# Performance work log

Hardware: AMD Instinct MI355X
Metric: run time of the kernel (lower is better)

## Reference

```python
import math
import jax, jax.numpy as jnp
import numpy as np
from jax import lax

# FPN anchor layout: 1024x768 image, strides {4,8,16,32,64}, 3 anchors/location
NUM_PER_LEVEL = (147456, 36864, 9216, 2304, 576)
A_TOTAL = sum(NUM_PER_LEVEL)
BATCH = 8
PRE_NMS_TOP_N = 1000   # testing
POST_NMS_TOP_N = 1000  # testing
NMS_THRESH = 0.7
SCORE_THRESH = 0.0
MIN_SIZE = 1.0
IMG_H, IMG_W = 768.0, 1024.0
BBOX_XFORM_CLIP = math.log(1000.0 / 16.0)


def setup_inputs() -> dict:
    key = jax.random.key(0)
    k1, k2, k3, k4, k5, k6 = jax.random.split(key, 6)
    objectness = jax.random.normal(k1, (BATCH, A_TOTAL), jnp.float32)
    pred_bbox_deltas = jax.random.normal(k2, (BATCH, A_TOTAL, 4), jnp.float32) * 0.2
    # valid anchor boxes (x1, y1, x2, y2)
    cx = jax.random.uniform(k3, (A_TOTAL,), jnp.float32) * IMG_W
    cy = jax.random.uniform(k4, (A_TOTAL,), jnp.float32) * IMG_H
    w = 16.0 + jax.random.uniform(k5, (A_TOTAL,), jnp.float32) * 176.0
    h = 16.0 + jax.random.uniform(k6, (A_TOTAL,), jnp.float32) * 176.0
    anchors = jnp.stack([cx - 0.5 * w, cy - 0.5 * h, cx + 0.5 * w, cy + 0.5 * h], -1)
    return {"objectness": objectness, "pred_bbox_deltas": pred_bbox_deltas, "anchors": anchors}


def _nms_image(boxes, scores, lvl, valid):
    """batched_nms (level-offset trick) + post-NMS top-k, fixed shapes.
    boxes [K,4], scores [K], lvl [K] int, valid [K] bool -> [POST_NMS_TOP_N, 5]"""
    K = boxes.shape[0]
    s = jnp.where(valid, scores, -1.0)
    order = jnp.argsort(-s)  # decreasing score (invalid last)
    b = boxes[order]
    s = s[order]
    v = valid[order]
    # offset boxes per level so cross-level boxes never overlap (torchvision batched_nms)
    offset = lvl[order].astype(b.dtype) * (jnp.max(lax.stop_gradient(boxes)) + 1.0)
    nb = lax.stop_gradient(b) + offset[:, None]
    area = (nb[:, 2] - nb[:, 0]) * (nb[:, 3] - nb[:, 1])
    lt = jnp.maximum(nb[:, None, :2], nb[None, :, :2])  # [K,K,2]
    rb = jnp.minimum(nb[:, None, 2:], nb[None, :, 2:])
    wh = jnp.clip(rb - lt, 0.0)
    inter = wh[..., 0] * wh[..., 1]
    iou = inter / jnp.maximum(area[:, None] + area[None, :] - inter, 1e-9)
    pos = jnp.arange(K)

    def body(keep, i):
        sup = keep[i] & (iou[i] > NMS_THRESH) & (pos > i)
        return keep & ~sup, None

    keep, _ = lax.scan(body, v, pos)
    masked = jnp.where(keep, s, -1.0)
    top_s, top_i = lax.top_k(masked, POST_NMS_TOP_N)  # kept, decreasing score
    sel_b = b[top_i]
    ok = top_s > -0.5
    sel_b = jnp.where(ok[:, None], sel_b, 0.0)
    top_s = jnp.where(ok, top_s, 0.0)
    return jnp.concatenate([sel_b, top_s[:, None]], axis=-1)


def reference(objectness, pred_bbox_deltas, anchors):
    # --- box decode (BoxCoder, weights (1,1,1,1)) ---
    wa = anchors[:, 2] - anchors[:, 0]
    ha = anchors[:, 3] - anchors[:, 1]
    cxa = anchors[:, 0] + 0.5 * wa
    cya = anchors[:, 1] + 0.5 * ha
    dx, dy = pred_bbox_deltas[..., 0], pred_bbox_deltas[..., 1]
    dw = jnp.minimum(pred_bbox_deltas[..., 2], BBOX_XFORM_CLIP)
    dh = jnp.minimum(pred_bbox_deltas[..., 3], BBOX_XFORM_CLIP)
    pcx = dx * wa + cxa
    pcy = dy * ha + cya
    pw = jnp.exp(dw) * wa
    ph = jnp.exp(dh) * ha
    proposals = jnp.stack(
        [pcx - 0.5 * pw, pcy - 0.5 * ph, pcx + 0.5 * pw, pcy + 0.5 * ph], axis=-1
    )  # [B, A, 4]

    # --- per-level pre-NMS top-k (_get_top_n_idx) ---
    levels = jnp.concatenate(
        [jnp.full((n,), i, jnp.int32) for i, n in enumerate(NUM_PER_LEVEL)]
    )
    idx_parts = []
    off = 0
    for n in NUM_PER_LEVEL:
        k = min(PRE_NMS_TOP_N, n)
        _, ti = lax.top_k(objectness[:, off:off + n], k)
        idx_parts.append(ti + off)
        off += n
    top_idx = jnp.concatenate(idx_parts, axis=1)  # [B, K]

    scores = jax.nn.sigmoid(jnp.take_along_axis(objectness, top_idx, axis=1))
    lvl = levels[top_idx]
    boxes = jnp.take_along_axis(proposals, top_idx[..., None], axis=1)  # [B,K,4]

    # --- clip to image ---
    x1 = jnp.clip(boxes[..., 0], 0.0, IMG_W)
    y1 = jnp.clip(boxes[..., 1], 0.0, IMG_H)
    x2 = jnp.clip(boxes[..., 2], 0.0, IMG_W)
    y2 = jnp.clip(boxes[..., 3], 0.0, IMG_H)
    boxes = jnp.stack([x1, y1, x2, y2], axis=-1)

    # remove_small_boxes + score threshold (as validity mask; fixed shapes)
    valid = ((x2 - x1) >= MIN_SIZE) & ((y2 - y1) >= MIN_SIZE) & (scores >= SCORE_THRESH)

    # --- per-image batched NMS + post-NMS top-k ---
    return jax.vmap(_nms_image)(boxes, scores, lvl, valid)  # [B, POST_NMS_TOP_N, 5]
```

## Files before the change

kernel.cpp:

```cpp
#include <hip/hip_runtime.h>
#include <math.h>

#pragma clang fp contract(off)

#define A_TOTAL 196416
#define BATCH 8
#define KTOT 4576
#define NLEV 5
#define MSPLIT 16
#define RCAP 6144
#define NPARTS 12

static __device__ const int d_aoff[NLEV] = {0, 147456, 184320, 193536, 195840};
static __device__ const int d_n[NLEV]    = {147456, 36864, 9216, 2304, 576};
static __device__ const int d_k[NLEV]    = {1000, 1000, 1000, 1000, 576};
static __device__ const int d_spl[NLEV]  = {8, 2, 1, 1, 1};
static __device__ const int d_bp[NLEV]   = {0, 8, 10, 11, 12};
static __device__ const int d_pb_l[13]    = {0,0,0,0,0,0,0,0,1,1,2,3,4};
static __device__ const int d_pb_part[13] = {0,1,2,3,4,5,6,7,0,1,0,0,0};

#define TM_IOU (0.699999988079071044921875 + 0x1p-25)

__device__ inline unsigned int mono(float f) {
  unsigned int u = __float_as_uint(f);
  return (u & 0x80000000u) ? ~u : (u | 0x80000000u);
}
__device__ inline float imono(unsigned int m) {
  return __uint_as_float((m & 0x80000000u) ? (m & 0x7FFFFFFFu) : ~m);
}

__device__ inline int cnt_gt(const float* A, int n, float s) {
  int lo = 0, hi = n;
  while (lo < hi) { int mid = (lo + hi) >> 1; if (A[mid] > s) lo = mid + 1; else hi = mid; }
  return lo;
}
__device__ inline int cnt_ge(const float* A, int n, float s) {
  int lo = 0, hi = n;
  while (lo < hi) { int mid = (lo + hi) >> 1; if (A[mid] >= s) lo = mid + 1; else hi = mid; }
  return lo;
}

__global__ __launch_bounds__(1024) void k_hist(const float* __restrict__ obj,
                                               int* __restrict__ hist_g,
                                               int* __restrict__ cnt_g,
                                               float* __restrict__ maxblk,
                                               float* __restrict__ out) {
  int blk = blockIdx.x;
  int tid = threadIdx.x;
  if (blk == 0) {
    for (int i = tid; i < 40 * NPARTS; i += 1024) maxblk[i] = 0.0f;
    for (int i = tid; i < 40; i += 1024) cnt_g[i] = 0;
  }
  int b = blk / 13, pb = blk % 13;
  if (pb == 0) {
    float* ob = out + (size_t)b * 5000;
    for (int i = tid; i < 5000; i += 1024) ob[i] = 0.0f;
  }
  int l = d_pb_l[pb], part = d_pb_part[pb];
  int slice = d_n[l] / d_spl[l];
  int start = d_aoff[l] + part * slice;
  const float4* p4 = (const float4*)(obj + (size_t)b * A_TOTAL + start);
  int s4 = slice >> 2;
  __shared__ int h[4096];
  for (int i = tid; i < 4096; i += 1024) h[i] = 0;
  __syncthreads();
  for (int i = tid; i < s4; i += 1024) {
    float4 v = p4[i];
    atomicAdd(&h[mono(v.x) >> 20], 1);
    atomicAdd(&h[mono(v.y) >> 20], 1);
    atomicAdd(&h[mono(v.z) >> 20], 1);
    atomicAdd(&h[mono(v.w) >> 20], 1);
  }
  __syncthreads();
  int* outp = hist_g + (size_t)blk * 4096;
  for (int i = tid; i < 4096; i += 1024) outp[i] = h[i];
}

__global__ __launch_bounds__(1024) void k_collect(const float* __restrict__ obj,
                                                  const int* __restrict__ hist_g,
                                                  int* __restrict__ cnt_g,
                                                  unsigned long long* __restrict__ cand_g) {
  int blk = blockIdx.x;
  int b = blk / 13, pb = blk % 13;
  int l = d_pb_l[pb], part = d_pb_part[pb];
  int bl = b * NLEV + l;
  const int k = d_k[l];
  int tid = threadIdx.x, lane = tid & 63;
  __shared__ int t[4096];
  __shared__ int grp[256];
  __shared__ unsigned int sP;
  __shared__ __align__(16) unsigned long long lbuf[RCAP];
  __shared__ int s_cnt, s_base;
  int parts = d_spl[l];
  const int* hb = hist_g + (size_t)(b * 13 + d_bp[l]) * 4096;
  for (int bin = tid; bin < 4096; bin += 1024) {
    int s = 0;
    for (int p = 0; p < parts; ++p) s += hb[p * 4096 + bin];
    t[bin] = s;
  }
  if (tid == 0) s_cnt = 0;
  __syncthreads();
  if (tid < 256) {
    int s = 0;
    for (int j = 0; j < 16; ++j) s += t[tid * 16 + j];
    grp[tid] = s;
  }
  __syncthreads();
  if (tid == 0) {
    int cum = 0, g, d;
    for (g = 255; g >= 0; --g) {
      if (cum + grp[g] >= k) break;
      cum += grp[g];
    }
    for (d = 15; d >= 0; --d) {
      int c = t[g * 16 + d];
      if (cum + c >= k) break;
      cum += c;
    }
    sP = (unsigned int)(g * 16 + d);
  }
  __syncthreads();
  unsigned int P = sP;
  int slice = d_n[l] / parts;
  int start = d_aoff[l] + part * slice;
  const float4* p4 = (const float4*)(obj + (size_t)b * A_TOTAL + start);
  int s4 = slice >> 2;
  int lbase = part * slice;
  for (int i = tid; i < s4; i += 1024) {
    float4 v = p4[i];
    unsigned int a[4] = {mono(v.x), mono(v.y), mono(v.z), mono(v.w)};
    bool q0 = (a[0] >> 20) >= P, q1 = (a[1] >> 20) >= P;
    bool q2 = (a[2] >> 20) >= P, q3 = (a[3] >> 20) >= P;
    if (__ballot(q0 | q1 | q2 | q3)) {
      bool qs[4] = {q0, q1, q2, q3};
#pragma unroll
      for (int c = 0; c < 4; ++c) {
        unsigned long long mb = __ballot(qs[c]);
        if (mb) {
          int base;
          if (lane == 0) base = atomicAdd(&s_cnt, __popcll(mb));
          base = __shfl(base, 0);
          if (qs[c]) {
            int slot = base + __popcll(mb & ((1ull << lane) - 1ull));
            if (slot < RCAP) {
              int idx = lbase + 4 * i + c;
              lbuf[slot] = ((unsigned long long)a[c] << 32) |
                           (unsigned int)(~(unsigned int)idx);
            }
          }
        }
      }
    }
  }
  __syncthreads();
  int cnt = min(s_cnt, RCAP);
  if (tid == 0) s_base = atomicAdd(&cnt_g[bl], cnt);
  __syncthreads();
  int base = s_base;
  for (int i = tid; i < cnt; i += 1024) {
    int slot = base + i;
    if (slot < RCAP) cand_g[(size_t)bl * RCAP + slot] = lbuf[i];
  }
}

__device__ inline float decode_emit(unsigned long long e, int rank, int b,
                                    int k, int aoff, int bl,
                                    const float* __restrict__ deltas,
                                    const float* __restrict__ anchors,
                                    float* __restrict__ sc0,
                                    float4* __restrict__ box0) {
  if (rank >= k) return 0.0f;
  unsigned int k32 = (unsigned int)(e >> 32);
  unsigned int idx = ~(unsigned int)(e & 0xFFFFFFFFull);
  float o = imono(k32);
  int gidx = aoff + (int)idx;
  const float* dl = deltas + ((size_t)b * A_TOTAL + gidx) * 4;
  const float* an = anchors + (size_t)gidx * 4;
  float a0 = an[0], a1 = an[1], a2 = an[2], a3 = an[3];
  float wa = a2 - a0, ha = a3 - a1;
  float cxa = a0 + 0.5f * wa, cya = a1 + 0.5f * ha;
  float dx = dl[0], dy = dl[1];
  const float CLIPV = 4.135166556742356f;
  float dw = fminf(dl[2], CLIPV), dh = fminf(dl[3], CLIPV);
  float pcx = dx * wa + cxa;
  float pcy = dy * ha + cya;
  float pw = (float)exp((double)dw) * wa;
  float ph = (float)exp((double)dh) * ha;
  float x1 = pcx - 0.5f * pw, y1 = pcy - 0.5f * ph;
  float x2 = pcx + 0.5f * pw, y2 = pcy + 0.5f * ph;
  x1 = fminf(fmaxf(x1, 0.0f), 1024.0f);
  x2 = fminf(fmaxf(x2, 0.0f), 1024.0f);
  y1 = fminf(fmaxf(y1, 0.0f), 768.0f);
  y2 = fminf(fmaxf(y2, 0.0f), 768.0f);
  float s = (float)(1.0 / (1.0 + exp(-(double)o)));
  bool valid = ((x2 - x1) >= 1.0f) && ((y2 - y1) >= 1.0f) && (s >= 0.0f);
  sc0[bl * 1024 + rank] = valid ? s : -1.0f;
  box0[bl * 1024 + rank] = make_float4(x1, y1, x2, y2);
  return fmaxf(fmaxf(x1, y1), fmaxf(x2, y2));
}

__global__ __launch_bounds__(256) void k_rankdec(const unsigned long long* __restrict__ cand_g,
                                                 const int* __restrict__ cnt_g,
                                                 const float* __restrict__ deltas,
                                                 const float* __restrict__ anchors,
                                                 float* __restrict__ sc0,
                                                 float4* __restrict__ box0,
                                                 float* __restrict__ maxblk) {
  int bl = blockIdx.x / NPARTS, part = blockIdx.x % NPARTS;
  int b = bl / NLEV, l = bl % NLEV;
  const int k = d_k[l], aoff = d_aoff[l];
  int cnt = min(cnt_g[bl], RCAP);
  if (part * 512 >= cnt) return;
  __shared__ __align__(16) unsigned long long cb[RCAP];
  __shared__ unsigned int s_max;
  int tid = threadIdx.x;
  if (tid == 0) s_max = 0u;
  const unsigned long long* src = cand_g + (size_t)bl * RCAP;
  {
    const ulonglong2* s2 = (const ulonglong2*)src;
    ulonglong2* d2 = (ulonglong2*)cb;
    int n2 = cnt >> 1;
    for (int i = tid; i < n2; i += 256) d2[i] = s2[i];
    if ((cnt & 1) && tid == 0) cb[cnt - 1] = src[cnt - 1];
  }
  __syncthreads();
  int i0 = part * 512 + tid, i1 = i0 + 256;
  unsigned long long e0 = ~0ull, e1 = ~0ull;
  if (i0 < cnt) e0 = cb[i0];
  if (i1 < cnt) e1 = cb[i1];
  int r0 = 0, r1 = 0;
  int nc2 = cnt >> 1;
  const ulonglong2* c2 = (const ulonglong2*)cb;
  for (int j = 0; j < nc2; ++j) {
    ulonglong2 v = c2[j];
    r0 += (v.x > e0) + (v.y > e0);
    r1 += (v.x > e1) + (v.y > e1);
  }
  if (cnt & 1) {
    unsigned long long v = cb[cnt - 1];
    r0 += (v > e0);
    r1 += (v > e1);
  }
  float mx = 0.0f;
  if (i0 < cnt) mx = fmaxf(mx, decode_emit(e0, r0, b, k, aoff, bl, deltas, anchors, sc0, box0));
  if (i1 < cnt) mx = fmaxf(mx, decode_emit(e1, r1, b, k, aoff, bl, deltas, anchors, sc0, box0));
#pragma unroll
  for (int s = 1; s < 64; s <<= 1) mx = fmaxf(mx, __shfl_xor(mx, s));
  if ((tid & 63) == 0) atomicMax(&s_max, __float_as_uint(mx));
  __syncthreads();
  if (tid == 0) maxblk[blockIdx.x] = __uint_as_float(s_max);
}

__global__ __launch_bounds__(1024) void k_mask(const float* __restrict__ sc0,
                                               const float4* __restrict__ box0,
                                               const float* __restrict__ maxblk,
                                               float* __restrict__ lvlsc,
                                               float4* __restrict__ lvlraw,
                                               int* __restrict__ g_V,
                                               unsigned long long* __restrict__ masks) {
  int blk = blockIdx.x;
  int bl = blk / MSPLIT, part = blk % MSPLIT;
  int b = bl / NLEV, l = bl % NLEV;
  const int k = d_k[l];
  int tid = threadIdx.x, lane = tid & 63, w = tid >> 6;
  __shared__ float4 lbox[1024];
  __shared__ float s_mv;
  __shared__ int s_wcnt[16];
  if (w == 0) {
    float v = 0.0f;
    for (int i = lane; i < NLEV * NPARTS; i += 64)
      v = fmaxf(v, maxblk[b * (NLEV * NPARTS) + i]);
#pragma unroll
    for (int s = 1; s < 64; s <<= 1) v = fmaxf(v, __shfl_xor(v, s));
    if (lane == 0) s_mv = v;
  }
  bool in = tid < k;
  float s = in ? sc0[bl * 1024 + tid] : -1.0f;
  bool valid = in && (s >= 0.0f);
  unsigned long long mb = __ballot(valid);
  if (lane == 0) s_wcnt[w] = __popcll(mb);
  __syncthreads();
  int pre = 0;
  for (int ww = 0; ww < w; ++ww) pre += s_wcnt[ww];
  int j = pre + __popcll(mb & ((1ull << lane) - 1ull));
  int V = 0;
  for (int ww = 0; ww < 16; ++ww) V += s_wcnt[ww];
  float off = (float)l * (s_mv + 1.0f);
  if (valid) {
    float4 bx = box0[bl * 1024 + tid];
    lbox[j] = make_float4(bx.x + off, bx.y + off, bx.z + off, bx.w + off);
    if (part == 0) {
      lvlsc[bl * 1024 + j] = s;
      lvlraw[bl * 1024 + j] = bx;
    }
  }
  if (part == 0 && tid == 0) g_V[bl] = V;
  __syncthreads();
  int row0 = part * 64;
  if (row0 >= V) return;
  int i = row0 + lane;
  if (i >= V) return;
  float4 bb = lbox[i];
  float ba = (bb.z - bb.x) * (bb.w - bb.y);
  unsigned long long bits = 0ull;
  int jbase = w * 64;
  if (jbase + 63 > i && jbase < V) {
    int jhi = min(64, V - jbase);
    for (int jo = 0; jo < jhi; ++jo) {
      int jj = jbase + jo;
      float4 cb = lbox[jj];
      float ca = (cb.z - cb.x) * (cb.w - cb.y);
      float xx1 = fmaxf(bb.x, cb.x), yy1 = fmaxf(bb.y, cb.y);
      float xx2 = fminf(bb.z, cb.z), yy2 = fminf(bb.w, cb.w);
      float wd = fmaxf(xx2 - xx1, 0.0f), ht = fmaxf(yy2 - yy1, 0.0f);
      float inter = wd * ht;
      float denom = fmaxf(ba + ca - inter, 1e-9f);
      if ((jj > i) && ((double)inter >= TM_IOU * (double)denom)) bits |= (1ull << jo);
    }
  }
  masks[((size_t)bl * 16 + w) * 1024 + i] = bits;
}

__global__ __launch_bounds__(1024) void k_scan(const unsigned long long* __restrict__ masks,
                                               const int* __restrict__ g_V,
                                               const float* __restrict__ lvlsc,
                                               float* __restrict__ ksc_g,
                                               int* __restrict__ kj_g,
                                               int* __restrict__ K_g) {
  int bl = blockIdx.x;
  int tid = threadIdx.x, lane = tid & 63, w = tid >> 6;
  int V = g_V[bl];
  const int nch = (V + 63) / 64;
  const unsigned long long* M = masks + (size_t)bl * 16 * 1024;
  __shared__ unsigned long long s_remv[16];
  __shared__ unsigned long long s_D[2][72];
  __shared__ unsigned long long s_dw;
  __shared__ int s_wcnt[16];
  if (tid < 16) s_remv[tid] = ~0ull;
  int base_w = w * 64;
  unsigned long long init_w;
  if (V <= base_w) init_w = ~0ull;
  else if (V >= base_w + 64) init_w = 0ull;
  else init_w = (~0ull) << (V - base_w);
  if (w == 0 && nch > 0) s_D[0][lane] = (lane < V) ? M[lane] : 0ull;
  if (tid < 8) { s_D[0][64 + tid] = 0ull; s_D[1][64 + tid] = 0ull; }
  unsigned long long acc = 0ull;
  unsigned long long val_next = 0ull;
  if (w > 0 && w < nch && lane < V) val_next = M[(size_t)w * 1024 + lane];
  __syncthreads();

  for (int c = 0; c < nch; ++c) {
    unsigned long long val = val_next;
    val_next = 0ull;
    int rn = 64 * (c + 1) + lane;
    if (w > c + 1 && w < nch && rn < V) val_next = M[(size_t)w * 1024 + rn];
    if (w == c) {
      unsigned long long red = acc;
#pragma unroll
      for (int s = 1; s < 64; s <<= 1) red |= __shfl_xor(red, s);
      unsigned long long dw = init_w | red;
      const unsigned long long* D = s_D[c & 1];
      unsigned long long pb[8];
#pragma unroll
      for (int u = 0; u < 8; ++u) pb[u] = D[u];
#pragma unroll
      for (int g = 0; g < 8; ++g) {
#pragma unroll
        for (int u = 0; u < 8; ++u) {
          int jj = g * 8 + u;
          if (!((dw >> jj) & 1ull)) dw |= pb[u];
          pb[u] = D[jj + 8];
        }
      }
      if (lane == 0) { s_dw = dw; s_remv[c] = dw; }
    }
    if (w == c + 1 && w < nch) {
      int rr = 64 * (c + 1) + lane;
      s_D[(c + 1) & 1][lane] = (rr < V) ? M[(size_t)(c + 1) * 1024 + rr] : 0ull;
    }
    __syncthreads();
    if (w > c && w < nch) {
      unsigned long long kept = ~s_dw;
      if ((kept >> lane) & 1ull) acc |= val;
    }
    __syncthreads();
  }

  unsigned long long kb = ~s_remv[w];
  bool kept = ((kb >> lane) & 1ull) != 0ull;
  unsigned long long mb = __ballot(kept);
  if (lane == 0) s_wcnt[w] = __popcll(mb);
  __syncthreads();
  int pre = 0;
  for (int ww = 0; ww < w; ++ww) pre += s_wcnt[ww];
  int r = pre + __popcll(mb & ((1ull << lane) - 1ull));
  if (kept) {
    ksc_g[bl * 1024 + r] = lvlsc[bl * 1024 + tid];
    kj_g[bl * 1024 + r] = tid;
  }
  if (tid == 0) {
    int t = 0;
    for (int ww = 0; ww < 16; ++ww) t += s_wcnt[ww];
    K_g[bl] = t;
  }
}

__global__ __launch_bounds__(1024) void k_merge(const float* __restrict__ ksc_g,
                                                const int* __restrict__ kj_g,
                                                const int* __restrict__ K_g,
                                                const float4* __restrict__ lvlraw,
                                                float* __restrict__ out) {
  int blk = blockIdx.x;
  int b = blk / NLEV, l = blk % NLEV;
  int tid = threadIdx.x;
  __shared__ float ksc[NLEV * 1024];
  __shared__ int sK[NLEV];
  if (tid < NLEV) sK[tid] = K_g[b * NLEV + tid];
  __syncthreads();
  int K[NLEV];
  for (int l2 = 0; l2 < NLEV; ++l2) K[l2] = sK[l2];
  for (int l2 = 0; l2 < NLEV; ++l2) {
    for (int i = tid; i < K[l2]; i += 1024)
      ksc[l2 * 1024 + i] = ksc_g[(size_t)(b * NLEV + l2) * 1024 + i];
  }
  __syncthreads();
  if (tid < K[l]) {
    float s = ksc[l * 1024 + tid];
    int rank = tid;
    for (int l2 = 0; l2 < NLEV; ++l2) {
      if (l2 == l) continue;
      const float* A = ksc + l2 * 1024;
      rank += (l2 < l) ? cnt_ge(A, K[l2], s) : cnt_gt(A, K[l2], s);
    }
    if (rank < 1000) {
      int j = kj_g[(size_t)(b * NLEV + l) * 1024 + tid];
      float4 bx = lvlraw[(size_t)(b * NLEV + l) * 1024 + j];
      float* op = out + (size_t)b * 5000 + (size_t)rank * 5;
      op[0] = bx.x; op[1] = bx.y; op[2] = bx.z; op[3] = bx.w; op[4] = s;
    }
  }
}

extern "C" void kernel_launch(void* const* d_in, const int* in_sizes, int n_in,
                              void* d_out, int out_size, void* d_ws, size_t ws_size,
                              hipStream_t stream) {
  const float* obj     = (const float*)d_in[0];
  const float* deltas  = (const float*)d_in[1];
  const float* anchors = (const float*)d_in[2];
  float* out = (float*)d_out;

  char* p = (char*)d_ws;
  float4* box0   = (float4*)p; p += (size_t)40 * 1024 * sizeof(float4);
  float4* lvlraw = (float4*)p; p += (size_t)40 * 1024 * sizeof(float4);
  unsigned long long* cand_g = (unsigned long long*)p; p += (size_t)40 * RCAP * 8;
  unsigned long long* masks  = (unsigned long long*)p; p += (size_t)40 * 16 * 1024 * 8;
  int*   hist_g = (int*)p;   p += (size_t)104 * 4096 * 4;
  int*   cnt_g  = (int*)p;   p += 40 * 4;
  float* maxblk = (float*)p; p += (size_t)40 * NPARTS * 4;
  float* sc0    = (float*)p; p += (size_t)40 * 1024 * 4;
  float* lvlsc  = (float*)p; p += (size_t)40 * 1024 * 4;
  int*   g_V    = (int*)p;   p += 40 * 4;
  float* ksc_g  = (float*)p; p += (size_t)40 * 1024 * 4;
  int*   kj_g   = (int*)p;   p += (size_t)40 * 1024 * 4;
  int*   K_g    = (int*)p;   p += 40 * 4;

  hipLaunchKernelGGL(k_hist, dim3(BATCH * 13), dim3(1024), 0, stream,
                     obj, hist_g, cnt_g, maxblk, out);
  hipLaunchKernelGGL(k_collect, dim3(BATCH * 13), dim3(1024), 0, stream,
                     obj, hist_g, cnt_g, cand_g);
  hipLaunchKernelGGL(k_rankdec, dim3(BATCH * NLEV * NPARTS), dim3(256), 0, stream,
                     cand_g, cnt_g, deltas, anchors, sc0, box0, maxblk);
  hipLaunchKernelGGL(k_mask, dim3(BATCH * NLEV * MSPLIT), dim3(1024), 0, stream,
                     sc0, box0, maxblk, lvlsc, lvlraw, g_V, masks);
  hipLaunchKernelGGL(k_scan, dim3(BATCH * NLEV), dim3(1024), 0, stream,
                     masks, g_V, lvlsc, ksc_g, kj_g, K_g);
  hipLaunchKernelGGL(k_merge, dim3(BATCH * NLEV), dim3(1024), 0, stream,
                     ksc_g, kj_g, K_g, lvlraw, out);
}
```

Before: 197.3 us.

## Run NMS mask scan in a single wavefront and parallelize histogram threshold search

Rewrites the NMS suppression scan so one 64-lane wavefront per (image, level) handles all 16 column words in registers. This removes the two block-wide barriers per 64-row chunk and the cross-wave shared-memory handoff. Separately, the serial single-thread search for the top-k histogram threshold bin is replaced by wave-level prefix scans and max-reductions over 64 lanes. The single-wave scan issues more global loads per lane (16 per chunk) and raises register pressure through the acc/val/keepw arrays, with less memory parallelism than the old 16-wave block.

After: 221.9 us. +12.5%, slower.

```diff
diff --git a/kernel.cpp b/kernel.cpp
--- a/kernel.cpp
+++ b/kernel.cpp
@@ -106,18 +106,45 @@
     grp[tid] = s;
   }
   __syncthreads();
-  if (tid == 0) {
-    int cum = 0, g, d;
-    for (g = 255; g >= 0; --g) {
-      if (cum + grp[g] >= k) break;
-      cum += grp[g];
-    }
-    for (d = 15; d >= 0; --d) {
-      int c = t[g * 16 + d];
-      if (cum + c >= k) break;
-      cum += c;
-    }
-    sP = (unsigned int)(g * 16 + d);
+  if (tid < 64) {
+    int g0 = grp[4 * tid], g1 = grp[4 * tid + 1];
+    int g2 = grp[4 * tid + 2], g3 = grp[4 * tid + 3];
+    int q = g0 + g1 + g2 + g3;
+    int x = q;
+#pragma unroll
+    for (int off = 1; off < 64; off <<= 1) {
+      int y = __shfl_down(x, off);
+      if (tid + off < 64) x += y;
+    }
+    int Qn = x - q;
+    int best = -1;
+    if (x >= k) best = 4 * tid;
+    if (g1 + g2 + g3 + Qn >= k) best = 4 * tid + 1;
+    if (g2 + g3 + Qn >= k) best = 4 * tid + 2;
+    if (g3 + Qn >= k) best = 4 * tid + 3;
+#pragma unroll
+    for (int off = 1; off < 64; off <<= 1) best = max(best, __shfl_xor(best, off));
+    int gstar = best;
+    int partl = 0;
+    if (4 * tid > gstar) partl += g0;
+    if (4 * tid + 1 > gstar) partl += g1;
+    if (4 * tid + 2 > gstar) partl += g2;
+    if (4 * tid + 3 > gstar) partl += g3;
+#pragma unroll
+    for (int off = 1; off < 64; off <<= 1) partl += __shfl_xor(partl, off);
+    int cum = partl;
+    int tb = (tid < 16) ? t[gstar * 16 + tid] : 0;
+    int Tx = tb;
+#pragma unroll
+    for (int off = 1; off < 16; off <<= 1) {
+      int y = __shfl_down(Tx, off);
+      if (tid + off < 16) Tx += y;
+    }
+    int bestd = -1;
+    if (tid < 16 && cum + Tx >= k) bestd = tid;
+#pragma unroll
+    for (int off = 1; off < 64; off <<= 1) bestd = max(bestd, __shfl_xor(bestd, off));
+    if (tid == 0) sP = (unsigned int)(gstar * 16 + bestd);
   }
   __syncthreads();
   unsigned int P = sP;
@@ -321,88 +348,84 @@
   masks[((size_t)bl * 16 + w) * 1024 + i] = bits;
 }
 
-__global__ __launch_bounds__(1024) void k_scan(const unsigned long long* __restrict__ masks,
-                                               const int* __restrict__ g_V,
-                                               const float* __restrict__ lvlsc,
-                                               float* __restrict__ ksc_g,
-                                               int* __restrict__ kj_g,
-                                               int* __restrict__ K_g) {
+__global__ __launch_bounds__(64) void k_scan(const unsigned long long* __restrict__ masks,
+                                             const int* __restrict__ g_V,
+                                             const float* __restrict__ lvlsc,
+                                             float* __restrict__ ksc_g,
+                                             int* __restrict__ kj_g,
+                                             int* __restrict__ K_g) {
   int bl = blockIdx.x;
-  int tid = threadIdx.x, lane = tid & 63, w = tid >> 6;
+  int lane = threadIdx.x;
   int V = g_V[bl];
-  const int nch = (V + 63) / 64;
+  int nch = (V + 63) >> 6;
   const unsigned long long* M = masks + (size_t)bl * 16 * 1024;
-  __shared__ unsigned long long s_remv[16];
-  __shared__ unsigned long long s_D[2][72];
-  __shared__ unsigned long long s_dw;
-  __shared__ int s_wcnt[16];
-  if (tid < 16) s_remv[tid] = ~0ull;
-  int base_w = w * 64;
-  unsigned long long init_w;
-  if (V <= base_w) init_w = ~0ull;
-  else if (V >= base_w + 64) init_w = 0ull;
-  else init_w = (~0ull) << (V - base_w);
-  if (w == 0 && nch > 0) s_D[0][lane] = (lane < V) ? M[lane] : 0ull;
-  if (tid < 8) { s_D[0][64 + tid] = 0ull; s_D[1][64 + tid] = 0ull; }
-  unsigned long long acc = 0ull;
-  unsigned long long val_next = 0ull;
-  if (w > 0 && w < nch && lane < V) val_next = M[(size_t)w * 1024 + lane];
-  __syncthreads();
+  __shared__ unsigned long long sD[2][72];
+  sD[0][lane] = (nch > 0 && lane < V) ? M[lane] : 0ull;
+  if (lane < 8) { sD[0][64 + lane] = 0ull; sD[1][64 + lane] = 0ull; }
+  unsigned long long acc[16], keepw[16];
+#pragma unroll
+  for (int w = 0; w < 16; ++w) { acc[w] = 0ull; keepw[w] = 0ull; }
 
   for (int c = 0; c < nch; ++c) {
-    unsigned long long val = val_next;
-    val_next = 0ull;
+    int r = 64 * c + lane;
+    bool rowok = (r < V);
+    unsigned long long val[16];
+#pragma unroll
+    for (int w = 0; w < 16; ++w) {
+      val[w] = 0ull;
+      if (w > c && w < nch && rowok) val[w] = M[(size_t)w * 1024 + r];
+    }
+    unsigned long long dnxt = 0ull;
     int rn = 64 * (c + 1) + lane;
-    if (w > c + 1 && w < nch && rn < V) val_next = M[(size_t)w * 1024 + rn];
-    if (w == c) {
-      unsigned long long red = acc;
-#pragma unroll
-      for (int s = 1; s < 64; s <<= 1) red |= __shfl_xor(red, s);
-      unsigned long long dw = init_w | red;
-      const unsigned long long* D = s_D[c & 1];
-      unsigned long long pb[8];
-#pragma unroll
-      for (int u = 0; u < 8; ++u) pb[u] = D[u];
-#pragma unroll
-      for (int g = 0; g < 8; ++g) {
-#pragma unroll
-        for (int u = 0; u < 8; ++u) {
-          int jj = g * 8 + u;
-          if (!((dw >> jj) & 1ull)) dw |= pb[u];
-          pb[u] = D[jj + 8];
-        }
+    if (c + 1 < nch && rn < V) dnxt = M[(size_t)(c + 1) * 1024 + rn];
+    unsigned long long red = 0ull;
+#pragma unroll
+    for (int w = 0; w < 16; ++w) if (w == c) red = acc[w];
+#pragma unroll
+    for (int s = 1; s < 64; s <<= 1) red |= __shfl_xor(red, s);
+    int base_r = 64 * c;
+    unsigned long long init_w =
+        (V >= base_r + 64) ? 0ull : ((~0ull) << (V - base_r));
+    unsigned long long dw = init_w | red;
+    const unsigned long long* D = sD[c & 1];
+    unsigned long long pb[8];
+#pragma unroll
+    for (int u = 0; u < 8; ++u) pb[u] = D[u];
+#pragma unroll
+    for (int g = 0; g < 8; ++g) {
+#pragma unroll
+      for (int u = 0; u < 8; ++u) {
+        int jj = g * 8 + u;
+        if (!((dw >> jj) & 1ull)) dw |= pb[u];
+        pb[u] = D[jj + 8];
       }
-      if (lane == 0) { s_dw = dw; s_remv[c] = dw; }
-    }
-    if (w == c + 1 && w < nch) {
-      int rr = 64 * (c + 1) + lane;
-      s_D[(c + 1) & 1][lane] = (rr < V) ? M[(size_t)(c + 1) * 1024 + rr] : 0ull;
-    }
-    __syncthreads();
-    if (w > c && w < nch) {
-      unsigned long long kept = ~s_dw;
-      if ((kept >> lane) & 1ull) acc |= val;
-    }
-    __syncthreads();
-  }
-
-  unsigned long long kb = ~s_remv[w];
-  bool kept = ((kb >> lane) & 1ull) != 0ull;
-  unsigned long long mb = __ballot(kept);
-  if (lane == 0) s_wcnt[w] = __popcll(mb);
-  __syncthreads();
-  int pre = 0;
-  for (int ww = 0; ww < w; ++ww) pre += s_wcnt[ww];
-  int r = pre + __popcll(mb & ((1ull << lane) - 1ull));
-  if (kept) {
-    ksc_g[bl * 1024 + r] = lvlsc[bl * 1024 + tid];
-    kj_g[bl * 1024 + r] = tid;
-  }
-  if (tid == 0) {
-    int t = 0;
-    for (int ww = 0; ww < 16; ++ww) t += s_wcnt[ww];
-    K_g[bl] = t;
-  }
+    }
+    sD[(c + 1) & 1][lane] = dnxt;
+    unsigned long long kept = ~dw;
+#pragma unroll
+    for (int w = 0; w < 16; ++w) if (w == c) keepw[w] = kept;
+    if (rowok && ((kept >> lane) & 1ull)) {
+#pragma unroll
+      for (int w = 0; w < 16; ++w)
+        if (w > c) acc[w] |= val[w];
+    }
+  }
+
+  int kbase = 0;
+#pragma unroll
+  for (int w = 0; w < 16; ++w) {
+    unsigned long long kb = keepw[w];
+    if (kb) {
+      int idx = kbase + __popcll(kb & ((1ull << lane) - 1ull));
+      if ((kb >> lane) & 1ull) {
+        int row = w * 64 + lane;
+        ksc_g[bl * 1024 + idx] = lvlsc[bl * 1024 + row];
+        kj_g[bl * 1024 + idx] = row;
+      }
+      kbase += __popcll(kb);
+    }
+  }
+  if (lane == 0) K_g[bl] = kbase;
 }
 
 __global__ __launch_bounds__(1024) void k_merge(const float* __restrict__ ksc_g,
@@ -472,7 +495,7 @@
                      cand_g, cnt_g, deltas, anchors, sc0, box0, maxblk);
   hipLaunchKernelGGL(k_mask, dim3(BATCH * NLEV * MSPLIT), dim3(1024), 0, stream,
                      sc0, box0, maxblk, lvlsc, lvlraw, g_V, masks);
-  hipLaunchKernelGGL(k_scan, dim3(BATCH * NLEV), dim3(1024), 0, stream,
+  hipLaunchKernelGGL(k_scan, dim3(BATCH * NLEV), dim3(64), 0, stream,
                      masks, g_V, lvlsc, ksc_g, kj_g, K_g);
   hipLaunchKernelGGL(k_merge, dim3(BATCH * NLEV), dim3(1024), 0, stream,
                      ksc_g, kj_g, K_g, lvlraw, out);
```

## Replace O(n^2) candidate ranking with bucket sort plus in-bucket ranking

Applied to the files above, without the earlier changes.

The rank-and-decode kernel used to compare every candidate against all others, split across 12 blocks per image-level. It now uses one 1024-thread block per image-level that histograms candidates on their top 12 key bits, builds suffix offsets, scatters them into buckets, and ranks each candidate only within its bucket, decoding only those ranked below k. The threshold search in the collect kernel is also parallelised with wavefront scans instead of a single-thread loop. The trade-off is far fewer blocks (40), which may underuse the GPU, and skewed buckets could make the in-bucket ranking costly.

After: 236.1 us. 19.7% more time.

```diff
diff --git a/kernel.cpp b/kernel.cpp
--- a/kernel.cpp
+++ b/kernel.cpp
@@ -9,7 +9,6 @@
 #define NLEV 5
 #define MSPLIT 16
 #define RCAP 6144
-#define NPARTS 12
 
 static __device__ const int d_aoff[NLEV] = {0, 147456, 184320, 193536, 195840};
 static __device__ const int d_n[NLEV]    = {147456, 36864, 9216, 2304, 576};
@@ -48,8 +47,7 @@
   int blk = blockIdx.x;
   int tid = threadIdx.x;
   if (blk == 0) {
-    for (int i = tid; i < 40 * NPARTS; i += 1024) maxblk[i] = 0.0f;
-    for (int i = tid; i < 40; i += 1024) cnt_g[i] = 0;
+    for (int i = tid; i < 40; i += 1024) { maxblk[i] = 0.0f; cnt_g[i] = 0; }
   }
   int b = blk / 13, pb = blk % 13;
   if (pb == 0) {
@@ -106,18 +104,45 @@
     grp[tid] = s;
   }
   __syncthreads();
-  if (tid == 0) {
-    int cum = 0, g, d;
-    for (g = 255; g >= 0; --g) {
-      if (cum + grp[g] >= k) break;
-      cum += grp[g];
-    }
-    for (d = 15; d >= 0; --d) {
-      int c = t[g * 16 + d];
-      if (cum + c >= k) break;
-      cum += c;
-    }
-    sP = (unsigned int)(g * 16 + d);
+  if (tid < 64) {
+    int g0 = grp[4 * tid], g1 = grp[4 * tid + 1];
+    int g2 = grp[4 * tid + 2], g3 = grp[4 * tid + 3];
+    int q = g0 + g1 + g2 + g3;
+    int x = q;
+#pragma unroll
+    for (int off = 1; off < 64; off <<= 1) {
+      int y = __shfl_down(x, off);
+      if (tid + off < 64) x += y;
+    }
+    int Qn = x - q;
+    int best = -1;
+    if (x >= k) best = 4 * tid;
+    if (g1 + g2 + g3 + Qn >= k) best = 4 * tid + 1;
+    if (g2 + g3 + Qn >= k) best = 4 * tid + 2;
+    if (g3 + Qn >= k) best = 4 * tid + 3;
+#pragma unroll
+    for (int off = 1; off < 64; off <<= 1) best = max(best, __shfl_xor(best, off));
+    int gstar = best;
+    int partl = 0;
+    if (4 * tid > gstar) partl += g0;
+    if (4 * tid + 1 > gstar) partl += g1;
+    if (4 * tid + 2 > gstar) partl += g2;
+    if (4 * tid + 3 > gstar) partl += g3;
+#pragma unroll
+    for (int off = 1; off < 64; off <<= 1) partl += __shfl_xor(partl, off);
+    int cum = partl;
+    int tb = (tid < 16) ? t[gstar * 16 + tid] : 0;
+    int Tx = tb;
+#pragma unroll
+    for (int off = 1; off < 16; off <<= 1) {
+      int y = __shfl_down(Tx, off);
+      if (tid + off < 16) Tx += y;
+    }
+    int bestd = -1;
+    if (tid < 16 && cum + Tx >= k) bestd = tid;
+#pragma unroll
+    for (int off = 1; off < 64; off <<= 1) bestd = max(bestd, __shfl_xor(bestd, off));
+    if (tid == 0) sP = (unsigned int)(gstar * 16 + bestd);
   }
   __syncthreads();
   unsigned int P = sP;
@@ -199,56 +224,71 @@
   return fmaxf(fmaxf(x1, y1), fmaxf(x2, y2));
 }
 
-__global__ __launch_bounds__(256) void k_rankdec(const unsigned long long* __restrict__ cand_g,
-                                                 const int* __restrict__ cnt_g,
-                                                 const float* __restrict__ deltas,
-                                                 const float* __restrict__ anchors,
-                                                 float* __restrict__ sc0,
-                                                 float4* __restrict__ box0,
-                                                 float* __restrict__ maxblk) {
-  int bl = blockIdx.x / NPARTS, part = blockIdx.x % NPARTS;
+__global__ __launch_bounds__(1024) void k_rankdec(const unsigned long long* __restrict__ cand_g,
+                                                  const int* __restrict__ cnt_g,
+                                                  const float* __restrict__ deltas,
+                                                  const float* __restrict__ anchors,
+                                                  float* __restrict__ sc0,
+                                                  float4* __restrict__ box0,
+                                                  float* __restrict__ maxblk) {
+  int bl = blockIdx.x;
   int b = bl / NLEV, l = bl % NLEV;
   const int k = d_k[l], aoff = d_aoff[l];
   int cnt = min(cnt_g[bl], RCAP);
-  if (part * 512 >= cnt) return;
-  __shared__ __align__(16) unsigned long long cb[RCAP];
+  int tid = threadIdx.x, lane = tid & 63, w = tid >> 6;
+  __shared__ int h[4096], sfx[4096], offs[4096];
+  __shared__ __align__(16) unsigned long long sorted[RCAP];
+  __shared__ int s_wsum[16];
   __shared__ unsigned int s_max;
-  int tid = threadIdx.x;
   if (tid == 0) s_max = 0u;
+  for (int i = tid; i < 4096; i += 1024) h[i] = 0;
+  __syncthreads();
   const unsigned long long* src = cand_g + (size_t)bl * RCAP;
-  {
-    const ulonglong2* s2 = (const ulonglong2*)src;
-    ulonglong2* d2 = (ulonglong2*)cb;
-    int n2 = cnt >> 1;
-    for (int i = tid; i < n2; i += 256) d2[i] = s2[i];
-    if ((cnt & 1) && tid == 0) cb[cnt - 1] = src[cnt - 1];
-  }
-  __syncthreads();
-  int i0 = part * 512 + tid, i1 = i0 + 256;
-  unsigned long long e0 = ~0ull, e1 = ~0ull;
-  if (i0 < cnt) e0 = cb[i0];
-  if (i1 < cnt) e1 = cb[i1];
-  int r0 = 0, r1 = 0;
-  int nc2 = cnt >> 1;
-  const ulonglong2* c2 = (const ulonglong2*)cb;
-  for (int j = 0; j < nc2; ++j) {
-    ulonglong2 v = c2[j];
-    r0 += (v.x > e0) + (v.y > e0);
-    r1 += (v.x > e1) + (v.y > e1);
-  }
-  if (cnt & 1) {
-    unsigned long long v = cb[cnt - 1];
-    r0 += (v > e0);
-    r1 += (v > e1);
-  }
+  for (int i = tid; i < cnt; i += 1024)
+    atomicAdd(&h[(unsigned int)(src[i] >> 52)], 1);
+  __syncthreads();
+  int t4 = tid * 4;
+  int h0 = h[t4], h1 = h[t4 + 1], h2 = h[t4 + 2], h3 = h[t4 + 3];
+  int mysum = h0 + h1 + h2 + h3;
+  int x = mysum;
+#pragma unroll
+  for (int off = 1; off < 64; off <<= 1) {
+    int y = __shfl_down(x, off);
+    if (lane + off < 64) x += y;
+  }
+  if (lane == 0) s_wsum[w] = x;
+  __syncthreads();
+  int wsuf = 0;
+  for (int ww = w + 1; ww < 16; ++ww) wsuf += s_wsum[ww];
+  int excl = (x - mysum) + wsuf;
+  sfx[t4 + 3] = excl;
+  sfx[t4 + 2] = excl + h3;
+  sfx[t4 + 1] = excl + h3 + h2;
+  sfx[t4]     = excl + h3 + h2 + h1;
+  offs[t4] = sfx[t4]; offs[t4 + 1] = sfx[t4 + 1];
+  offs[t4 + 2] = sfx[t4 + 2]; offs[t4 + 3] = sfx[t4 + 3];
+  __syncthreads();
+  for (int i = tid; i < cnt; i += 1024) {
+    unsigned long long e = src[i];
+    int pos = atomicAdd(&offs[(unsigned int)(e >> 52)], 1);
+    sorted[pos] = e;
+  }
+  __syncthreads();
   float mx = 0.0f;
-  if (i0 < cnt) mx = fmaxf(mx, decode_emit(e0, r0, b, k, aoff, bl, deltas, anchors, sc0, box0));
-  if (i1 < cnt) mx = fmaxf(mx, decode_emit(e1, r1, b, k, aoff, bl, deltas, anchors, sc0, box0));
+  for (int p = tid; p < cnt; p += 1024) {
+    unsigned long long e = sorted[p];
+    unsigned int bin = (unsigned int)(e >> 52);
+    int s0 = sfx[bin], s1 = s0 + h[bin];
+    int rank = s0;
+    for (int j = s0; j < s1; ++j) rank += (sorted[j] > e);
+    if (rank < k)
+      mx = fmaxf(mx, decode_emit(e, rank, b, k, aoff, bl, deltas, anchors, sc0, box0));
+  }
 #pragma unroll
   for (int s = 1; s < 64; s <<= 1) mx = fmaxf(mx, __shfl_xor(mx, s));
-  if ((tid & 63) == 0) atomicMax(&s_max, __float_as_uint(mx));
-  __syncthreads();
-  if (tid == 0) maxblk[blockIdx.x] = __uint_as_float(s_max);
+  if (lane == 0) atomicMax(&s_max, __float_as_uint(mx));
+  __syncthreads();
+  if (tid == 0) maxblk[bl] = __uint_as_float(s_max);
 }
 
 __global__ __launch_bounds__(1024) void k_mask(const float* __restrict__ sc0,
@@ -267,9 +307,7 @@
   __shared__ float s_mv;
   __shared__ int s_wcnt[16];
   if (w == 0) {
-    float v = 0.0f;
-    for (int i = lane; i < NLEV * NPARTS; i += 64)
-      v = fmaxf(v, maxblk[b * (NLEV * NPARTS) + i]);
+    float v = (lane < NLEV) ? maxblk[b * NLEV + lane] : 0.0f;
 #pragma unroll
     for (int s = 1; s < 64; s <<= 1) v = fmaxf(v, __shfl_xor(v, s));
     if (lane == 0) s_mv = v;
@@ -456,7 +494,7 @@
   unsigned long long* masks  = (unsigned long long*)p; p += (size_t)40 * 16 * 1024 * 8;
   int*   hist_g = (int*)p;   p += (size_t)104 * 4096 * 4;
   int*   cnt_g  = (int*)p;   p += 40 * 4;
-  float* maxblk = (float*)p; p += (size_t)40 * NPARTS * 4;
+  float* maxblk = (float*)p; p += 40 * 4;
   float* sc0    = (float*)p; p += (size_t)40 * 1024 * 4;
   float* lvlsc  = (float*)p; p += (size_t)40 * 1024 * 4;
   int*   g_V    = (int*)p;   p += 40 * 4;
@@ -468,7 +506,7 @@
                      obj, hist_g, cnt_g, maxblk, out);
   hipLaunchKernelGGL(k_collect, dim3(BATCH * 13), dim3(1024), 0, stream,
                      obj, hist_g, cnt_g, cand_g);
-  hipLaunchKernelGGL(k_rankdec, dim3(BATCH * NLEV * NPARTS), dim3(256), 0, stream,
+  hipLaunchKernelGGL(k_rankdec, dim3(BATCH * NLEV), dim3(1024), 0, stream,
                      cand_g, cnt_g, deltas, anchors, sc0, box0, maxblk);
   hipLaunchKernelGGL(k_mask, dim3(BATCH * NLEV * MSPLIT), dim3(1024), 0, stream,
                      sc0, box0, maxblk, lvlsc, lvlraw, g_V, masks);
```

## Fuse scan and merge kernels with per-image spin barrier; parallelize threshold search

Applied to the files above, without the earlier changes.

Merges the k_scan and k_merge kernels into one k_tail kernel. The five level-blocks of each image now meet at a global atomic counter with a spin-wait, which removes one kernel launch and the round trip of intermediate data through a separate kernel. The bin-threshold search in k_collect also changes from a serial single-thread loop to a wavefront-parallel prefix scan using shuffles. This relies on all 40 blocks being resident at the same time to avoid deadlock, and it adds atomic reads and writes for the cross-block data exchange.

Result: slower. 201.3 us (+2.0%).

```diff
diff --git a/kernel.cpp b/kernel.cpp
--- a/kernel.cpp
+++ b/kernel.cpp
@@ -44,12 +44,14 @@
                                                int* __restrict__ hist_g,
                                                int* __restrict__ cnt_g,
                                                float* __restrict__ maxblk,
+                                               int* __restrict__ done,
                                                float* __restrict__ out) {
   int blk = blockIdx.x;
   int tid = threadIdx.x;
   if (blk == 0) {
     for (int i = tid; i < 40 * NPARTS; i += 1024) maxblk[i] = 0.0f;
     for (int i = tid; i < 40; i += 1024) cnt_g[i] = 0;
+    if (tid < BATCH) done[tid] = 0;
   }
   int b = blk / 13, pb = blk % 13;
   if (pb == 0) {
@@ -106,18 +108,45 @@
     grp[tid] = s;
   }
   __syncthreads();
-  if (tid == 0) {
-    int cum = 0, g, d;
-    for (g = 255; g >= 0; --g) {
-      if (cum + grp[g] >= k) break;
-      cum += grp[g];
-    }
-    for (d = 15; d >= 0; --d) {
-      int c = t[g * 16 + d];
-      if (cum + c >= k) break;
-      cum += c;
-    }
-    sP = (unsigned int)(g * 16 + d);
+  if (tid < 64) {
+    int g0 = grp[4 * tid], g1 = grp[4 * tid + 1];
+    int g2 = grp[4 * tid + 2], g3 = grp[4 * tid + 3];
+    int q = g0 + g1 + g2 + g3;
+    int x = q;
+#pragma unroll
+    for (int off = 1; off < 64; off <<= 1) {
+      int y = __shfl_down(x, off);
+      if (tid + off < 64) x += y;
+    }
+    int Qn = x - q;
+    int best = -1;
+    if (x >= k) best = 4 * tid;
+    if (g1 + g2 + g3 + Qn >= k) best = 4 * tid + 1;
+    if (g2 + g3 + Qn >= k) best = 4 * tid + 2;
+    if (g3 + Qn >= k) best = 4 * tid + 3;
+#pragma unroll
+    for (int off = 1; off < 64; off <<= 1) best = max(best, __shfl_xor(best, off));
+    int gstar = best;
+    int partl = 0;
+    if (4 * tid > gstar) partl += g0;
+    if (4 * tid + 1 > gstar) partl += g1;
+    if (4 * tid + 2 > gstar) partl += g2;
+    if (4 * tid + 3 > gstar) partl += g3;
+#pragma unroll
+    for (int off = 1; off < 64; off <<= 1) partl += __shfl_xor(partl, off);
+    int cum = partl;
+    int tb = (tid < 16) ? t[gstar * 16 + tid] : 0;
+    int Tx = tb;
+#pragma unroll
+    for (int off = 1; off < 16; off <<= 1) {
+      int y = __shfl_down(Tx, off);
+      if (tid + off < 16) Tx += y;
+    }
+    int bestd = -1;
+    if (tid < 16 && cum + Tx >= k) bestd = tid;
+#pragma unroll
+    for (int off = 1; off < 64; off <<= 1) bestd = max(bestd, __shfl_xor(bestd, off));
+    if (tid == 0) sP = (unsigned int)(gstar * 16 + bestd);
   }
   __syncthreads();
   unsigned int P = sP;
@@ -321,13 +350,17 @@
   masks[((size_t)bl * 16 + w) * 1024 + i] = bits;
 }
 
-__global__ __launch_bounds__(1024) void k_scan(const unsigned long long* __restrict__ masks,
+__global__ __launch_bounds__(1024) void k_tail(const unsigned long long* __restrict__ masks,
                                                const int* __restrict__ g_V,
                                                const float* __restrict__ lvlsc,
                                                float* __restrict__ ksc_g,
                                                int* __restrict__ kj_g,
-                                               int* __restrict__ K_g) {
+                                               int* __restrict__ K_g,
+                                               int* __restrict__ done,
+                                               const float4* __restrict__ lvlraw,
+                                               float* __restrict__ out) {
   int bl = blockIdx.x;
+  int b = bl / NLEV, l = bl % NLEV;
   int tid = threadIdx.x, lane = tid & 63, w = tid >> 6;
   int V = g_V[bl];
   const int nch = (V + 63) / 64;
@@ -395,33 +428,36 @@
   for (int ww = 0; ww < w; ++ww) pre += s_wcnt[ww];
   int r = pre + __popcll(mb & ((1ull << lane) - 1ull));
   if (kept) {
-    ksc_g[bl * 1024 + r] = lvlsc[bl * 1024 + tid];
+    atomicExch(&ksc_g[bl * 1024 + r], lvlsc[bl * 1024 + tid]);
     kj_g[bl * 1024 + r] = tid;
   }
+  int Kown = 0;
+  for (int ww = 0; ww < 16; ++ww) Kown += s_wcnt[ww];
+  if (tid == 0) atomicExch(&K_g[bl], Kown);
+  __threadfence();
+  __syncthreads();
+  if (tid == 0) atomicAdd(&done[b], 1);
+
   if (tid == 0) {
-    int t = 0;
-    for (int ww = 0; ww < 16; ++ww) t += s_wcnt[ww];
-    K_g[bl] = t;
-  }
-}
-
-__global__ __launch_bounds__(1024) void k_merge(const float* __restrict__ ksc_g,
-                                                const int* __restrict__ kj_g,
-                                                const int* __restrict__ K_g,
-                                                const float4* __restrict__ lvlraw,
-                                                float* __restrict__ out) {
-  int blk = blockIdx.x;
-  int b = blk / NLEV, l = blk % NLEV;
-  int tid = threadIdx.x;
+    while (atomicAdd(&done[b], 0) < NLEV) __builtin_amdgcn_s_sleep(8);
+  }
+  __syncthreads();
   __shared__ float ksc[NLEV * 1024];
   __shared__ int sK[NLEV];
-  if (tid < NLEV) sK[tid] = K_g[b * NLEV + tid];
+  if (tid < NLEV) sK[tid] = atomicAdd(&K_g[b * NLEV + tid], 0);
   __syncthreads();
   int K[NLEV];
   for (int l2 = 0; l2 < NLEV; ++l2) K[l2] = sK[l2];
   for (int l2 = 0; l2 < NLEV; ++l2) {
-    for (int i = tid; i < K[l2]; i += 1024)
-      ksc[l2 * 1024 + i] = ksc_g[(size_t)(b * NLEV + l2) * 1024 + i];
+    float* dst = ksc + l2 * 1024;
+    if (l2 == l) {
+      for (int i = tid; i < K[l2]; i += 1024)
+        dst[i] = ksc_g[(size_t)bl * 1024 + i];
+    } else {
+      float* srcp = ksc_g + (size_t)(b * NLEV + l2) * 1024;
+      for (int i = tid; i < K[l2]; i += 1024)
+        dst[i] = atomicAdd(&srcp[i], 0.0f);
+    }
   }
   __syncthreads();
   if (tid < K[l]) {
@@ -433,8 +469,8 @@
       rank += (l2 < l) ? cnt_ge(A, K[l2], s) : cnt_gt(A, K[l2], s);
     }
     if (rank < 1000) {
-      int j = kj_g[(size_t)(b * NLEV + l) * 1024 + tid];
-      float4 bx = lvlraw[(size_t)(b * NLEV + l) * 1024 + j];
+      int j = kj_g[(size_t)bl * 1024 + tid];
+      float4 bx = lvlraw[(size_t)bl * 1024 + j];
       float* op = out + (size_t)b * 5000 + (size_t)rank * 5;
       op[0] = bx.x; op[1] = bx.y; op[2] = bx.z; op[3] = bx.w; op[4] = s;
     }
@@ -463,17 +499,16 @@
   float* ksc_g  = (float*)p; p += (size_t)40 * 1024 * 4;
   int*   kj_g   = (int*)p;   p += (size_t)40 * 1024 * 4;
   int*   K_g    = (int*)p;   p += 40 * 4;
+  int*   done   = (int*)p;   p += BATCH * 4;
 
   hipLaunchKernelGGL(k_hist, dim3(BATCH * 13), dim3(1024), 0, stream,
-                     obj, hist_g, cnt_g, maxblk, out);
+                     obj, hist_g, cnt_g, maxblk, done, out);
   hipLaunchKernelGGL(k_collect, dim3(BATCH * 13), dim3(1024), 0, stream,
                      obj, hist_g, cnt_g, cand_g);
   hipLaunchKernelGGL(k_rankdec, dim3(BATCH * NLEV * NPARTS), dim3(256), 0, stream,
                      cand_g, cnt_g, deltas, anchors, sc0, box0, maxblk);
   hipLaunchKernelGGL(k_mask, dim3(BATCH * NLEV * MSPLIT), dim3(1024), 0, stream,
                      sc0, box0, maxblk, lvlsc, lvlraw, g_V, masks);
-  hipLaunchKernelGGL(k_scan, dim3(BATCH * NLEV), dim3(1024), 0, stream,
-                     masks, g_V, lvlsc, ksc_g, kj_g, K_g);
-  hipLaunchKernelGGL(k_merge, dim3(BATCH * NLEV), dim3(1024), 0, stream,
-                     ksc_g, kj_g, K_g, lvlraw, out);
-}
+  hipLaunchKernelGGL(k_tail, dim3(BATCH * NLEV), dim3(1024), 0, stream,
+                     masks, g_V, lvlsc, ksc_g, kj_g, K_g, done, lvlraw, out);
+}
```
